# Kernel optimization log

Hardware: AMD Instinct MI355X
Metric: run time of the kernel (lower is better)

The kernel has to match this reference:

```python
import jax, jax.numpy as jnp
import numpy as np
from jax import lax

V, D, H, K, B, T = 32000, 300, 300, 9, 64, 512


def _lstm_dir(x, w_ih, w_hh, b_ih, b_hh, h0, c0):
    # x: [B, T, D]; torch gate order: i, f, g, o
    def step(carry, xt):
        h, c = carry
        gates = xt @ w_ih.T + h @ w_hh.T + b_ih + b_hh  # [B, 4H]
        i, f, g, o = jnp.split(gates, 4, axis=-1)
        i, f, o = jax.nn.sigmoid(i), jax.nn.sigmoid(f), jax.nn.sigmoid(o)
        g = jnp.tanh(g)
        c = f * c + i * g
        h = o * jnp.tanh(c)
        return (h, c), h

    xs = jnp.transpose(x, (1, 0, 2))  # [T, B, D]
    _, hs = lax.scan(step, (h0, c0), xs)
    return jnp.transpose(hs, (1, 0, 2))  # [B, T, H]


def _emissions(tokens, emb, w_ih_f, w_hh_f, b_ih_f, b_hh_f,
               w_ih_b, w_hh_b, b_ih_b, b_hh_b, h0, c0, w_out, b_out):
    x = emb[tokens]  # [B, T, D]
    hf = _lstm_dir(x, w_ih_f, w_hh_f, b_ih_f, b_hh_f, h0[0], c0[0])
    hb = _lstm_dir(jnp.flip(x, axis=1), w_ih_b, w_hh_b, b_ih_b, b_hh_b, h0[1], c0[1])
    hb = jnp.flip(hb, axis=1)
    out = jnp.concatenate([hf, hb], axis=-1)  # [B, T, 2H]
    return out @ w_out.T + b_out  # [B, T, K]


def _crf_nll(emissions, tags, mask, start_t, end_t, trans):
    # torchcrf: -sum_b log p(tags | emissions)
    e = jnp.transpose(emissions, (1, 0, 2))  # [T, B, K]
    tg = tags.T                               # [T, B]
    m = mask.T.astype(emissions.dtype)        # [T, B]
    bidx = jnp.arange(tags.shape[0])
    # numerator: gold path score
    num = start_t[tg[0]] + e[0][bidx, tg[0]]
    def nstep(carry, inp):
        et, tt, tp, mt = inp
        return carry + (trans[tp, tt] + et[bidx, tt]) * mt, None
    num, _ = lax.scan(nstep, num, (e[1:], tg[1:], tg[:-1], m[1:]))
    last_idx = mask.sum(axis=1).astype(jnp.int32) - 1
    last_tags = tags[bidx, last_idx]
    num = num + end_t[last_tags]
    # denominator: forward algorithm
    alpha = start_t + e[0]  # [B, K]
    def dstep(alpha, inp):
        et, mt = inp
        nxt = jax.scipy.special.logsumexp(alpha[:, :, None] + trans[None], axis=1) + et
        return jnp.where(mt[:, None] > 0, nxt, alpha), None
    alpha, _ = lax.scan(dstep, alpha, (e[1:], m[1:]))
    den = jax.scipy.special.logsumexp(alpha + end_t, axis=1)
    return -jnp.sum(num - den)


def _viterbi(emissions, mask, start_t, end_t, trans):
    e = jnp.transpose(emissions, (1, 0, 2))  # [T, B, K]
    m = mask.T                               # [T, B]
    score = start_t + e[0]                   # [B, K]
    def fstep(score, inp):
        et, mt = inp
        br = score[:, :, None] + trans[None]  # [B, K_prev, K_next]
        best = br.max(axis=1)
        idx = br.argmax(axis=1).astype(jnp.int32)  # [B, K]
        new = best + et
        return jnp.where(mt[:, None], new, score), idx
    score, history = lax.scan(fstep, score, (e[1:], m[1:]))  # history: [T-1, B, K]
    score = score + end_t
    last = jnp.argmax(score, axis=-1).astype(jnp.int32)  # [B]
    def bstep(tag, inp):
        idx_t, mt = inp
        prev = jnp.take_along_axis(idx_t, tag[:, None], axis=1)[:, 0]
        tag = jnp.where(mt, prev, tag)
        return tag, tag
    _, tags_rev = lax.scan(bstep, last, (history, m[1:]), reverse=True)  # [T-1, B]
    path = jnp.concatenate([tags_rev, last[None]], axis=0)  # [T, B]
    return path.T  # [B, T]


def setup_inputs() -> dict:
    key = jax.random.key(0)
    ks = jax.random.split(key, 20)
    s = 0.1
    emb = jax.random.normal(ks[0], (V, D), jnp.float32) * s
    emb = emb.at[0].set(0.0)  # padding_idx row
    inp = {
        "tokens": jax.random.randint(ks[1], (B, T), 0, V, jnp.int32),
        "tags": jax.random.randint(ks[2], (B, T), 0, K, jnp.int32),
        "mask": jnp.ones((B, T), jnp.bool_),
        "emb": emb,
        "w_ih_f": jax.random.normal(ks[3], (4 * H, D), jnp.float32) * s,
        "w_hh_f": jax.random.normal(ks[4], (4 * H, H), jnp.float32) * s,
        "b_ih_f": jax.random.normal(ks[5], (4 * H,), jnp.float32) * s,
        "b_hh_f": jax.random.normal(ks[6], (4 * H,), jnp.float32) * s,
        "w_ih_b": jax.random.normal(ks[7], (4 * H, D), jnp.float32) * s,
        "w_hh_b": jax.random.normal(ks[8], (4 * H, H), jnp.float32) * s,
        "b_ih_b": jax.random.normal(ks[9], (4 * H,), jnp.float32) * s,
        "b_hh_b": jax.random.normal(ks[10], (4 * H,), jnp.float32) * s,
        "h0": jax.random.normal(ks[11], (2, B, H), jnp.float32),
        "c0": jax.random.normal(ks[12], (2, B, H), jnp.float32),
        "w_out": jax.random.normal(ks[13], (K, 2 * H), jnp.float32) * s,
        "b_out": jax.random.normal(ks[14], (K,), jnp.float32) * s,
        "start_t": jax.random.normal(ks[15], (K,), jnp.float32) * s,
        "end_t": jax.random.normal(ks[16], (K,), jnp.float32) * s,
        "trans": jax.random.normal(ks[17], (K, K), jnp.float32) * s,
    }
    return inp


def reference(tokens, tags, mask, emb, w_ih_f, w_hh_f, b_ih_f, b_hh_f,
              w_ih_b, w_hh_b, b_ih_b, b_hh_b, h0, c0, w_out, b_out,
              start_t, end_t, trans):
    feats = _emissions(tokens, emb, w_ih_f, w_hh_f, b_ih_f, b_hh_f,
                       w_ih_b, w_hh_b, b_ih_b, b_hh_b, h0, c0, w_out, b_out)
    paths = _viterbi(feats, mask, start_t, end_t, trans)
    loss = _crf_nll(feats, tags, mask, start_t, end_t, trans)
    return paths, loss
```

## Files before the change

### kernel.cpp

```cpp
#include <hip/hip_runtime.h>
#include <math.h>

#define NV 32000
#define ND 300
#define NH 300
#define NK 9
#define NB 64
#define NT 512

typedef short bf16x8 __attribute__((ext_vector_type(8)));
typedef float f32x4  __attribute__((ext_vector_type(4)));

__device__ inline short bf16r(float x) {
    return (short)((__float_as_uint(x) + 0x8000u) >> 16);
}

__device__ inline float tanh_fast(float x) {
    float e2 = __expf(2.f * x);
    return 1.f - 2.f / (e2 + 1.f);
}

__device__ inline void bar_lds() {
    asm volatile("s_waitcnt lgkmcnt(0)" ::: "memory");
    __builtin_amdgcn_s_barrier();
    asm volatile("" ::: "memory");
}

#define WB_OFF   0ull
#define WB_F     768000ull
#define E_OFF    (WB_OFF + WB_F)
#define E_SZ     ((unsigned long long)NT*NB*NK)
#define CBUF_OFF (E_OFF + E_SZ)
#define CBUF_SZ  (2ull*NB*NH)
#define HSLOT_OFF (CBUF_OFF + CBUF_SZ)
#define HSLOT_SZ  (2ull*2*NB*NH)
#define XP_OFF   (HSLOT_OFF + HSLOT_SZ)
#define XPC_SZ   (2ull*64*1200*64)

__global__ __launch_bounds__(256) void k_wcvt(
    const float* __restrict__ wihf, const float* __restrict__ wihb,
    const float* __restrict__ whhf, const float* __restrict__ whhb,
    short* __restrict__ dst)
{
    int i = blockIdx.x*256 + threadIdx.x;
    if (i >= 1536000) return;
    int d  = i / 384000;
    int r2 = i % 384000;
    int j  = r2 / 320, k = r2 % 320;
    const float* src = (d == 0) ? wihf : (d == 1) ? wihb : (d == 2) ? whhf : whhb;
    float v = (k < 300) ? src[(size_t)j*300 + k] : 0.f;
    dst[i] = bf16r(v);
}

__global__ __launch_bounds__(256) void k_xproj(
    const int* __restrict__ tokens, const float* __restrict__ emb,
    const short* __restrict__ wb16,
    const float* __restrict__ bif, const float* __restrict__ bhf,
    const float* __restrict__ bib, const float* __restrict__ bhb,
    float* __restrict__ xpc, int chunk)
{
    const int tid = threadIdx.x;
    const int w  = tid >> 6, L = tid & 63;
    const int lm = L & 15, lq = L >> 4;
    const int dir = blockIdx.z;
    const int m0 = blockIdx.x*128 + w*32;
    const int n0 = blockIdx.y*80;
    const int tbase = dir ? (448 - chunk*64) : (chunk*64);

    const float* arow[2];
#pragma unroll
    for (int mi = 0; mi < 2; ++mi) {
        int m = m0 + mi*16 + lm;
        int b = m >> 6, lt = m & 63;
        arow[mi] = emb + (size_t)tokens[b*512 + tbase + lt] * 300;
    }
    const short* brow[5];
#pragma unroll
    for (int ni = 0; ni < 5; ++ni) {
        int j = n0 + ni*16 + lm;
        brow[ni] = wb16 + ((size_t)dir*1200 + j)*320;
    }

    f32x4 acc[2][5];
#pragma unroll
    for (int mi = 0; mi < 2; ++mi)
#pragma unroll
        for (int ni = 0; ni < 5; ++ni)
#pragma unroll
            for (int r = 0; r < 4; ++r) acc[mi][ni][r] = 0.f;

    const float4 z4 = make_float4(0.f,0.f,0.f,0.f);
    for (int k0 = 0; k0 < 320; k0 += 32) {
        const int kk = k0 + lq*8;
        bf16x8 af[2], bf[5];
#pragma unroll
        for (int mi = 0; mi < 2; ++mi) {
            float4 f1 = (kk   < 300) ? *(const float4*)(arow[mi] + kk)     : z4;
            float4 f2 = (kk+4 < 300) ? *(const float4*)(arow[mi] + kk + 4) : z4;
            af[mi][0]=bf16r(f1.x); af[mi][1]=bf16r(f1.y); af[mi][2]=bf16r(f1.z); af[mi][3]=bf16r(f1.w);
            af[mi][4]=bf16r(f2.x); af[mi][5]=bf16r(f2.y); af[mi][6]=bf16r(f2.z); af[mi][7]=bf16r(f2.w);
        }
#pragma unroll
        for (int ni = 0; ni < 5; ++ni)
            bf[ni] = *(const bf16x8*)(brow[ni] + kk);
#pragma unroll
        for (int mi = 0; mi < 2; ++mi)
#pragma unroll
            for (int ni = 0; ni < 5; ++ni)
                acc[mi][ni] = __builtin_amdgcn_mfma_f32_16x16x32_bf16(
                                  af[mi], bf[ni], acc[mi][ni], 0, 0, 0);
    }

#pragma unroll
    for (int ni = 0; ni < 5; ++ni) {
        int j = n0 + ni*16 + lm;
        int g = j/300, rr = j%300;
        int slc = rr/20, ul = rr%20;
        float bias = dir ? (bib[j]+bhb[j]) : (bif[j]+bhf[j]);
#pragma unroll
        for (int mi = 0; mi < 2; ++mi) {
#pragma unroll
            for (int r = 0; r < 4; ++r) {
                int m = m0 + mi*16 + lq*4 + r;
                int b = m >> 6, lt = m & 63;
                int sp = dir ? (63 - lt) : lt;
                size_t idx = ((((size_t)dir*64 + sp)*8 + (b>>3))*15 + slc)*640
                           + (size_t)(b&7)*80 + g*20 + ul;
                xpc[idx] = acc[mi][ni][r] + bias;
            }
        }
    }
}

__global__ __launch_bounds__(256) void k_rnn(
    const float* __restrict__ xpc,
    const short* __restrict__ whh16,
    const float* __restrict__ h0,
    unsigned* hslot, float* __restrict__ cbuf,
    float* __restrict__ ev, const float* __restrict__ wout,
    int s_begin, int s_count, int full)
{
    extern __shared__ char lds_pad[];
    __shared__ __align__(16) short h_sh16[16*328];
    __shared__ __align__(16) float xp_sh[640];
    __shared__ __align__(16) float gates_sh[80*9];
    __shared__ __align__(16) float wo_sh[180];
    __shared__ __align__(16) float hloc[160];
    __shared__ __align__(16) float ev_loc[64*72];
    (void)lds_pad;

    const int tid = threadIdx.x;
    const int wv  = tid >> 6, L = tid & 63;
    const int lm  = L & 15, lq = L >> 4;
    const int dir = blockIdx.x / 120;
    const int rem = blockIdx.x % 120;
    const int sl  = rem / 8;
    const int gb  = rem % 8;
    const int u0  = sl * 20;

    const int tb = (wv == 0) ? 0 : (wv + 1);
    const int tn = (wv == 0) ? 2 : 1;

    bf16x8 A[2][10];
#pragma unroll 2
    for (int mt = 0; mt < 2; ++mt) {
        if (mt < tn) {
            int r = (tb + mt)*16 + lm;
            int grow = (r/20)*300 + u0 + (r%20);
            const short* wr = whh16 + ((size_t)dir*1200 + grow)*320;
#pragma unroll
            for (int ks = 0; ks < 10; ++ks)
                A[mt][ks] = *(const bf16x8*)(wr + ks*32 + lq*8);
        }
    }
    if (tid < 180) wo_sh[tid] = wout[(tid/20)*600 + dir*300 + u0 + (tid%20)];

    for (int i = tid; i < 16*328; i += 256) h_sh16[i] = 0;

    const bool isPW = (tid < 160);
    const int bl_p = tid/20, lu_p = tid%20;
    float c_reg = 0.f;
    if (isPW) c_reg = cbuf[((size_t)dir*NB + gb*8 + bl_p)*NH + u0 + lu_p];

    auto xaddr = [&](int s) -> const float* {
        const float* xb; int sp;
        if (full) { xb = xpc + (size_t)(s >> 6)*XPC_SZ; sp = s & 63; }
        else      { xb = xpc;                            sp = s - s_begin; }
        return xb + ((((size_t)dir*64 + sp)*8 + gb)*15 + sl)*640 + (size_t)tid*4;
    };
    float4 xpr;
    if (tid < 160) xpr = *(const float4*)xaddr(s_begin);

    bar_lds();

    for (int s = s_begin; s < s_begin + s_count; ++s) {
        unsigned vb[10];
        unsigned* hsrc = hslot + (((size_t)(s & 1)*2 + dir)*NB + gb*8)*NH;
        if (s > 0 && tid < 240) {
#pragma unroll
            for (int j = 0; j < 10; ++j) {
                int i = tid + 256*j;
                if (i < 2400)
                    vb[j] = __hip_atomic_load(hsrc + i, __ATOMIC_RELAXED,
                                              __HIP_MEMORY_SCOPE_AGENT);
            }
        }

        if (tid < 160) *(float4*)(&xp_sh[tid*4]) = xpr;
        if (tid < 160 && (s + 1) < s_begin + s_count)
            xpr = *(const float4*)xaddr(s + 1);

        if (s == 0) {
            const float* h0p = h0 + ((size_t)dir*NB + gb*8)*NH;
            for (int i = tid; i < 2400; i += 256)
                h_sh16[(i/300)*328 + (i%300)] = bf16r(h0p[i]);
        } else if (tid < 240) {
            const unsigned tg = (unsigned)s & 0xFFFFu;
            bool ok = false;
            while (!ok) {
                ok = true;
#pragma unroll
                for (int j = 0; j < 10; ++j) {
                    int i = tid + 256*j;
                    if (i < 2400 && (vb[j] >> 16) != tg) {
                        ok = false;
                        vb[j] = __hip_atomic_load(hsrc + i, __ATOMIC_RELAXED,
                                                  __HIP_MEMORY_SCOPE_AGENT);
                    }
                }
            }
#pragma unroll
            for (int j = 0; j < 10; ++j) {
                int i = tid + 256*j;
                if (i < 2400)
                    h_sh16[(i/300)*328 + (i%300)] = (short)(vb[j] & 0xFFFFu);
            }
        }
        bar_lds();

        {
            bf16x8 Bf[10];
#pragma unroll
            for (int ks = 0; ks < 10; ++ks)
                Bf[ks] = *(const bf16x8*)(h_sh16 + lm*328 + ks*32 + lq*8);
            f32x4 acc0, acc1;
#pragma unroll 2
            for (int mt = 0; mt < 2; ++mt) {
                if (mt < tn) {
#pragma unroll
                    for (int r = 0; r < 4; ++r) { acc0[r] = 0.f; acc1[r] = 0.f; }
#pragma unroll
                    for (int ks = 0; ks < 5; ++ks)
                        acc0 = __builtin_amdgcn_mfma_f32_16x16x32_bf16(
                                   A[mt][ks], Bf[ks], acc0, 0, 0, 0);
#pragma unroll
                    for (int ks = 5; ks < 10; ++ks)
                        acc1 = __builtin_amdgcn_mfma_f32_16x16x32_bf16(
                                   A[mt][ks], Bf[ks], acc1, 0, 0, 0);
                    if (lm < 8) {
#pragma unroll
                        for (int r = 0; r < 4; ++r)
                            gates_sh[((tb+mt)*16 + lq*4 + r)*9 + lm] = acc0[r] + acc1[r];
                    }
                }
            }
        }
        bar_lds();

        if (isPW) {
            float G[4];
#pragma unroll
            for (int g = 0; g < 4; ++g)
                G[g] = xp_sh[bl_p*80 + g*20 + lu_p] + gates_sh[(g*20 + lu_p)*9 + bl_p];
            float ig = 1.f/(1.f+__expf(-G[0]));
            float fg = 1.f/(1.f+__expf(-G[1]));
            float gg = tanh_fast(G[2]);
            float og = 1.f/(1.f+__expf(-G[3]));
            c_reg = fg*c_reg + ig*gg;
            float h = og*tanh_fast(c_reg);
            unsigned hb = (__float_as_uint(h) + 0x8000u) >> 16;
            unsigned pk = (((unsigned)(s+1) & 0xFFFFu) << 16) | hb;
            __hip_atomic_store(
                &hslot[(((size_t)((s+1)&1)*2 + dir)*NB + gb*8 + bl_p)*NH + u0 + lu_p],
                pk, __ATOMIC_RELAXED, __HIP_MEMORY_SCOPE_AGENT);
            hloc[bl_p*20 + lu_p] = h;
        }
        bar_lds();

        const int widx = (s - s_begin) & 63;
        if (tid < 72) {
            int b = tid/9, k = tid%9;
            float a = 0.f;
#pragma unroll
            for (int u = 0; u < 20; ++u) a += hloc[b*20+u]*wo_sh[k*20+u];
            ev_loc[widx*72 + tid] = a;
        }

        if (widx == 63) {
            bar_lds();
            const int sbase = s - 63;
            for (int i = tid; i < 64*72; i += 256) {
                int wi = i / 72, j = i % 72;
                int bb = j / 9, kk = j % 9;
                int tt = dir ? (511 - (sbase + wi)) : (sbase + wi);
                atomicAdd(&ev[((size_t)tt*NB + gb*8 + bb)*NK + kk], ev_loc[i]);
            }
        }
    }

    if (isPW) cbuf[((size_t)dir*NB + gb*8 + bl_p)*NH + u0 + lu_p] = c_reg;
}

#define BT_C 14
#define BT_L 37

__global__ __launch_bounds__(128) void k_crf(
    const float* __restrict__ ev, const int* __restrict__ tags,
    const float* __restrict__ start_t, const float* __restrict__ end_t,
    const float* __restrict__ trans, const float* __restrict__ bout,
    float* __restrict__ out)
{
    __shared__ __align__(16) float ex_a[12];
    __shared__ __align__(16) float ex_v[12];
    __shared__ int hist_sh[511*NK];
    __shared__ int fmap[BT_C*NK];
    __shared__ int entry_sh[BT_C];
    __shared__ int last_sh;

    const int b = blockIdx.x, tid = threadIdx.x;
    const int wv = tid >> 6, ln = tid & 63;

    if (wv == 0) {
        float part = 0.f;
        for (int t = ln; t < NT; t += 64) {
            int tc = tags[b*NT + t];
            float e = ev[((size_t)t*NB + b)*NK + tc] + bout[tc];
            float pre = (t == 0) ? start_t[tc] : trans[tags[b*NT + t - 1]*9 + tc];
            part += pre + e;
        }
        if (ln == 63) part += end_t[tags[b*NT + NT - 1]];
#pragma unroll
        for (int off = 32; off > 0; off >>= 1)
            part += __shfl_down(part, off, 64);
        const float num = part;

        if (ln < 9) {
            const int kc = ln;
            float Tc[9];
#pragma unroll
            for (int kp = 0; kp < 9; ++kp) Tc[kp] = __expf(trans[kp*9 + kc]);
            const float bo = bout[kc];
            ex_a[kc] = start_t[kc] + ev[(size_t)b*NK + kc] + bo;
            float etn = ev[((size_t)1*NB + b)*NK + kc] + bo;

            for (int t = 1; t < NT; ++t) {
                float et = etn;
                if (t + 1 < NT) etn = ev[((size_t)(t+1)*NB + b)*NK + kc] + bo;

                float4 s0 = *(const float4*)(&ex_a[0]);
                float4 s1 = *(const float4*)(&ex_a[4]);
                float  a8 = ex_a[8];
                float a0=s0.x,a1=s0.y,a2=s0.z,a3=s0.w,a4=s1.x,a5=s1.y,a6=s1.z,a7=s1.w;

                float M = fmaxf(fmaxf(fmaxf(a0,a1),fmaxf(a2,a3)),
                                fmaxf(fmaxf(a4,a5),fmaxf(a6,a7)));
                M = fmaxf(M, a8);
                float s =        __expf(a0-M)*Tc[0];
                s = fmaf(__expf(a1-M), Tc[1], s);
                s = fmaf(__expf(a2-M), Tc[2], s);
                s = fmaf(__expf(a3-M), Tc[3], s);
                s = fmaf(__expf(a4-M), Tc[4], s);
                s = fmaf(__expf(a5-M), Tc[5], s);
                s = fmaf(__expf(a6-M), Tc[6], s);
                s = fmaf(__expf(a7-M), Tc[7], s);
                s = fmaf(__expf(a8-M), Tc[8], s);
                ex_a[kc] = M + __logf(s) + et;
            }

            if (ln == 0) {
                float M = -1e30f;
#pragma unroll
                for (int k = 0; k < 9; ++k) M = fmaxf(M, ex_a[k] + end_t[k]);
                float ls = 0.f;
#pragma unroll
                for (int k = 0; k < 9; ++k) ls += __expf(ex_a[k] + end_t[k] - M);
                float den = M + __logf(ls);
                atomicAdd(out + NB*NT, den - num);
            }
        }
    } else {
        if (ln < 9) {
            const int kc = ln;
            float Tc[9];
#pragma unroll
            for (int kp = 0; kp < 9; ++kp) Tc[kp] = trans[kp*9 + kc];
            const float bo = bout[kc];
            ex_v[kc] = start_t[kc] + ev[(size_t)b*NK + kc] + bo;
            float etn = ev[((size_t)1*NB + b)*NK + kc] + bo;

            for (int t = 1; t < NT; ++t) {
                float et = etn;
                if (t + 1 < NT) etn = ev[((size_t)(t+1)*NB + b)*NK + kc] + bo;

                float4 s0 = *(const float4*)(&ex_v[0]);
                float4 s1 = *(const float4*)(&ex_v[4]);
                float  a8 = ex_v[8];
                float a0=s0.x,a1=s0.y,a2=s0.z,a3=s0.w,a4=s1.x,a5=s1.y,a6=s1.z,a7=s1.w;

                float bv = a0 + Tc[0]; int arg = 0;
                float v;
                v = a1+Tc[1]; if (v > bv) { bv = v; arg = 1; }
                v = a2+Tc[2]; if (v > bv) { bv = v; arg = 2; }
                v = a3+Tc[3]; if (v > bv) { bv = v; arg = 3; }
                v = a4+Tc[4]; if (v > bv) { bv = v; arg = 4; }
                v = a5+Tc[5]; if (v > bv) { bv = v; arg = 5; }
                v = a6+Tc[6]; if (v > bv) { bv = v; arg = 6; }
                v = a7+Tc[7]; if (v > bv) { bv = v; arg = 7; }
                v = a8+Tc[8]; if (v > bv) { bv = v; arg = 8; }
                hist_sh[(t-1)*NK + kc] = arg;
                ex_v[kc] = bv + et;
            }

            if (ln == 0) {
                float best = -1e30f; int last = 0;
#pragma unroll
                for (int k = 0; k < 9; ++k) {
                    float v = ex_v[k] + end_t[k];
                    if (v > best) { best = v; last = k; }
                }
                last_sh = last;
            }
        }
    }

    __syncthreads();

    if (tid < BT_C*NK) {
        int c = tid / NK, s = tid % NK;
        int lo = c*BT_L, hi = min(511, lo + BT_L);
        int pos = s;
        for (int i = hi - 1; i >= lo; --i) pos = hist_sh[i*NK + pos];
        fmap[c*NK + s] = pos;
    }
    __syncthreads();
    if (tid == 0) {
        int e = last_sh;
        entry_sh[BT_C-1] = e;
        for (int c = BT_C - 2; c >= 0; --c) {
            e = fmap[(c+1)*NK + e];
            entry_sh[c] = e;
        }
    }
    __syncthreads();
    int* pout = (int*)out;
    if (tid < BT_C) {
        int c = tid;
        int lo = c*BT_L, hi = min(511, lo + BT_L);
        int pos = entry_sh[c];
        for (int i = hi - 1; i >= lo; --i) {
            pos = hist_sh[i*NK + pos];
            pout[b*NT + i] = pos;
        }
    }
    if (tid == 0) pout[b*NT + NT - 1] = last_sh;
}

extern "C" void kernel_launch(void* const* d_in, const int* in_sizes, int n_in,
                              void* d_out, int out_size, void* d_ws, size_t ws_size,
                              hipStream_t stream)
{
    (void)in_sizes; (void)n_in;

    const int*   tokens = (const int*)  d_in[0];
    const int*   tags   = (const int*)  d_in[1];
    const float* emb    = (const float*)d_in[3];
    const float* wihf   = (const float*)d_in[4];
    const float* whhf   = (const float*)d_in[5];
    const float* bihf   = (const float*)d_in[6];
    const float* bhhf   = (const float*)d_in[7];
    const float* wihb   = (const float*)d_in[8];
    const float* whhb   = (const float*)d_in[9];
    const float* bib    = (const float*)d_in[10];
    const float* bhhb   = (const float*)d_in[11];
    const float* h0     = (const float*)d_in[12];
    const float* c0     = (const float*)d_in[13];
    const float* wout   = (const float*)d_in[14];
    const float* bout   = (const float*)d_in[15];
    const float* startt = (const float*)d_in[16];
    const float* endt   = (const float*)d_in[17];
    const float* trans  = (const float*)d_in[18];

    float* ws    = (float*)d_ws;
    short* wb16  = (short*)(ws + WB_OFF);
    short* whh16 = wb16 + 768000;
    float* evp   = ws + E_OFF;
    float* cbuf  = ws + CBUF_OFF;
    unsigned* hslot = (unsigned*)(ws + HSLOT_OFF);
    float* xp    = ws + XP_OFF;
    float* out   = (float*)d_out;

    const size_t need_full = (XP_OFF + 8ull*XPC_SZ) * 4ull;
    const bool full = (ws_size >= need_full);

    (void)hipMemsetAsync(d_out, 0, (size_t)out_size * sizeof(float), stream);
    (void)hipMemsetAsync(evp, 0, (size_t)E_SZ * sizeof(float), stream);
    (void)hipMemcpyAsync(cbuf, c0, 2ull*NB*NH*sizeof(float), hipMemcpyDeviceToDevice, stream);

    k_wcvt<<<6000, 256, 0, stream>>>(wihf, wihb, whhf, whhb, wb16);

    if (full) {
        for (int c = 0; c < 8; ++c)
            k_xproj<<<dim3(32, 15, 2), 256, 0, stream>>>(
                tokens, emb, wb16, bihf, bhhf, bib, bhhb, xp + (size_t)c*XPC_SZ, c);
        k_rnn<<<240, 256, 81920, stream>>>(
            xp, whh16, h0, hslot, cbuf, evp, wout, 0, 512, 1);
    } else {
        for (int c = 0; c < 8; ++c) {
            k_xproj<<<dim3(32, 15, 2), 256, 0, stream>>>(
                tokens, emb, wb16, bihf, bhhf, bib, bhhb, xp, c);
            k_rnn<<<240, 256, 81920, stream>>>(
                xp, whh16, h0, hslot, cbuf, evp, wout, c*64, 64, 0);
        }
    }
    k_crf<<<64, 128, 0, stream>>>(evp, tags, startt, endt, trans, bout, out);
}
```

Before: 2.005 ms.

## Pre-convert embeddings to bf16 and always run chunked xproj/rnn launches

Adds a kernel converting the full embedding table to padded bf16 so the input projection loads bf16 rows directly instead of converting fp32 on the fly. The recurrent kernel is simplified: it always runs in 64-step chunks interleaved with projection launches, drops the xp register prefetch and the 80KB dynamic LDS padding, and emits emissions via per-step atomics instead of batched LDS staging. This trades conversion cost and more launches/atomics for simpler code and reduced per-element conversion work.

```diff
diff --git a/kernel.cpp b/kernel.cpp
--- a/kernel.cpp
+++ b/kernel.cpp
@@ -18,12 +18,6 @@
 __device__ inline float tanh_fast(float x) {
     float e2 = __expf(2.f * x);
     return 1.f - 2.f / (e2 + 1.f);
-}
-
-__device__ inline void bar_lds() {
-    asm volatile("s_waitcnt lgkmcnt(0)" ::: "memory");
-    __builtin_amdgcn_s_barrier();
-    asm volatile("" ::: "memory");
 }
 
 #define WB_OFF   0ull
@@ -36,6 +30,9 @@
 #define HSLOT_SZ  (2ull*2*NB*NH)
 #define XP_OFF   (HSLOT_OFF + HSLOT_SZ)
 #define XPC_SZ   (2ull*64*1200*64)
+#define EB_OFF   (XP_OFF + XPC_SZ)
+#define EB_SZ    (32000ull*320/2)
+#define WS_NEED_EB ((EB_OFF + EB_SZ)*4ull)
 
 __global__ __launch_bounds__(256) void k_wcvt(
     const float* __restrict__ wihf, const float* __restrict__ wihb,
@@ -52,8 +49,19 @@
     dst[i] = bf16r(v);
 }
 
+__global__ __launch_bounds__(256) void k_ecvt(
+    const float* __restrict__ emb, short* __restrict__ dst)
+{
+    int i = blockIdx.x*256 + threadIdx.x;
+    if (i >= 32000*320) return;
+    int row = i / 320, col = i % 320;
+    float v = (col < 300) ? emb[(size_t)row*300 + col] : 0.f;
+    dst[i] = bf16r(v);
+}
+
 __global__ __launch_bounds__(256) void k_xproj(
     const int* __restrict__ tokens, const float* __restrict__ emb,
+    const short* __restrict__ eb16, int use_eb,
     const short* __restrict__ wb16,
     const float* __restrict__ bif, const float* __restrict__ bhf,
     const float* __restrict__ bib, const float* __restrict__ bhb,
@@ -67,12 +75,12 @@
     const int n0 = blockIdx.y*80;
     const int tbase = dir ? (448 - chunk*64) : (chunk*64);
 
-    const float* arow[2];
+    int tok[2];
 #pragma unroll
     for (int mi = 0; mi < 2; ++mi) {
         int m = m0 + mi*16 + lm;
         int b = m >> 6, lt = m & 63;
-        arow[mi] = emb + (size_t)tokens[b*512 + tbase + lt] * 300;
+        tok[mi] = tokens[b*512 + tbase + lt];
     }
     const short* brow[5];
 #pragma unroll
@@ -89,26 +97,51 @@
 #pragma unroll
             for (int r = 0; r < 4; ++r) acc[mi][ni][r] = 0.f;
 
-    const float4 z4 = make_float4(0.f,0.f,0.f,0.f);
-    for (int k0 = 0; k0 < 320; k0 += 32) {
-        const int kk = k0 + lq*8;
-        bf16x8 af[2], bf[5];
-#pragma unroll
-        for (int mi = 0; mi < 2; ++mi) {
-            float4 f1 = (kk   < 300) ? *(const float4*)(arow[mi] + kk)     : z4;
-            float4 f2 = (kk+4 < 300) ? *(const float4*)(arow[mi] + kk + 4) : z4;
-            af[mi][0]=bf16r(f1.x); af[mi][1]=bf16r(f1.y); af[mi][2]=bf16r(f1.z); af[mi][3]=bf16r(f1.w);
-            af[mi][4]=bf16r(f2.x); af[mi][5]=bf16r(f2.y); af[mi][6]=bf16r(f2.z); af[mi][7]=bf16r(f2.w);
-        }
-#pragma unroll
-        for (int ni = 0; ni < 5; ++ni)
-            bf[ni] = *(const bf16x8*)(brow[ni] + kk);
-#pragma unroll
-        for (int mi = 0; mi < 2; ++mi)
+    if (use_eb) {
+        const short* arow[2];
+#pragma unroll
+        for (int mi = 0; mi < 2; ++mi) arow[mi] = eb16 + (size_t)tok[mi]*320;
+        for (int k0 = 0; k0 < 320; k0 += 32) {
+            const int kk = k0 + lq*8;
+            bf16x8 af[2], bf[5];
+#pragma unroll
+            for (int mi = 0; mi < 2; ++mi)
+                af[mi] = *(const bf16x8*)(arow[mi] + kk);
 #pragma unroll
             for (int ni = 0; ni < 5; ++ni)
-                acc[mi][ni] = __builtin_amdgcn_mfma_f32_16x16x32_bf16(
-                                  af[mi], bf[ni], acc[mi][ni], 0, 0, 0);
+                bf[ni] = *(const bf16x8*)(brow[ni] + kk);
+#pragma unroll
+            for (int mi = 0; mi < 2; ++mi)
+#pragma unroll
+                for (int ni = 0; ni < 5; ++ni)
+                    acc[mi][ni] = __builtin_amdgcn_mfma_f32_16x16x32_bf16(
+                                      af[mi], bf[ni], acc[mi][ni], 0, 0, 0);
+        }
+    } else {
+        const float* arow[2];
+#pragma unroll
+        for (int mi = 0; mi < 2; ++mi) arow[mi] = emb + (size_t)tok[mi]*300;
+        const float4 z4 = make_float4(0.f,0.f,0.f,0.f);
+        for (int k0 = 0; k0 < 320; k0 += 32) {
+            const int kk = k0 + lq*8;
+            bf16x8 af[2], bf[5];
+#pragma unroll
+            for (int mi = 0; mi < 2; ++mi) {
+                float4 f1 = (kk   < 300) ? *(const float4*)(arow[mi] + kk)     : z4;
+                float4 f2 = (kk+4 < 300) ? *(const float4*)(arow[mi] + kk + 4) : z4;
+                af[mi][0]=bf16r(f1.x); af[mi][1]=bf16r(f1.y); af[mi][2]=bf16r(f1.z); af[mi][3]=bf16r(f1.w);
+                af[mi][4]=bf16r(f2.x); af[mi][5]=bf16r(f2.y); af[mi][6]=bf16r(f2.z); af[mi][7]=bf16r(f2.w);
+            }
+#pragma unroll
+            for (int ni = 0; ni < 5; ++ni)
+                bf[ni] = *(const bf16x8*)(brow[ni] + kk);
+#pragma unroll
+            for (int mi = 0; mi < 2; ++mi)
+#pragma unroll
+                for (int ni = 0; ni < 5; ++ni)
+                    acc[mi][ni] = __builtin_amdgcn_mfma_f32_16x16x32_bf16(
+                                      af[mi], bf[ni], acc[mi][ni], 0, 0, 0);
+        }
     }
 
 #pragma unroll
@@ -138,16 +171,13 @@
     const float* __restrict__ h0,
     unsigned* hslot, float* __restrict__ cbuf,
     float* __restrict__ ev, const float* __restrict__ wout,
-    int s_begin, int s_count, int full)
+    int s_begin, int s_count)
 {
-    extern __shared__ char lds_pad[];
     __shared__ __align__(16) short h_sh16[16*328];
     __shared__ __align__(16) float xp_sh[640];
     __shared__ __align__(16) float gates_sh[80*9];
     __shared__ __align__(16) float wo_sh[180];
     __shared__ __align__(16) float hloc[160];
-    __shared__ __align__(16) float ev_loc[64*72];
-    (void)lds_pad;
 
     const int tid = threadIdx.x;
     const int wv  = tid >> 6, L = tid & 63;
@@ -182,18 +212,12 @@
     float c_reg = 0.f;
     if (isPW) c_reg = cbuf[((size_t)dir*NB + gb*8 + bl_p)*NH + u0 + lu_p];
 
-    auto xaddr = [&](int s) -> const float* {
-        const float* xb; int sp;
-        if (full) { xb = xpc + (size_t)(s >> 6)*XPC_SZ; sp = s & 63; }
-        else      { xb = xpc;                            sp = s - s_begin; }
-        return xb + ((((size_t)dir*64 + sp)*8 + gb)*15 + sl)*640 + (size_t)tid*4;
-    };
-    float4 xpr;
-    if (tid < 160) xpr = *(const float4*)xaddr(s_begin);
-
-    bar_lds();
+    __syncthreads();
 
     for (int s = s_begin; s < s_begin + s_count; ++s) {
+        const int t = dir ? (511 - s) : s;
+        const int sp = s - s_begin;
+
         unsigned vb[10];
         unsigned* hsrc = hslot + (((size_t)(s & 1)*2 + dir)*NB + gb*8)*NH;
         if (s > 0 && tid < 240) {
@@ -206,9 +230,10 @@
             }
         }
 
-        if (tid < 160) *(float4*)(&xp_sh[tid*4]) = xpr;
-        if (tid < 160 && (s + 1) < s_begin + s_count)
-            xpr = *(const float4*)xaddr(s + 1);
+        {
+            const float* xsrc = xpc + ((((size_t)dir*64 + sp)*8 + gb)*15 + sl)*640;
+            if (tid < 160) *(float4*)(&xp_sh[tid*4]) = *(const float4*)(xsrc + tid*4);
+        }
 
         if (s == 0) {
             const float* h0p = h0 + ((size_t)dir*NB + gb*8)*NH;
@@ -236,36 +261,32 @@
                     h_sh16[(i/300)*328 + (i%300)] = (short)(vb[j] & 0xFFFFu);
             }
         }
-        bar_lds();
+        __syncthreads();
 
         {
             bf16x8 Bf[10];
 #pragma unroll
             for (int ks = 0; ks < 10; ++ks)
                 Bf[ks] = *(const bf16x8*)(h_sh16 + lm*328 + ks*32 + lq*8);
-            f32x4 acc0, acc1;
+            f32x4 acc[2];
 #pragma unroll 2
             for (int mt = 0; mt < 2; ++mt) {
                 if (mt < tn) {
 #pragma unroll
-                    for (int r = 0; r < 4; ++r) { acc0[r] = 0.f; acc1[r] = 0.f; }
-#pragma unroll
-                    for (int ks = 0; ks < 5; ++ks)
-                        acc0 = __builtin_amdgcn_mfma_f32_16x16x32_bf16(
-                                   A[mt][ks], Bf[ks], acc0, 0, 0, 0);
-#pragma unroll
-                    for (int ks = 5; ks < 10; ++ks)
-                        acc1 = __builtin_amdgcn_mfma_f32_16x16x32_bf16(
-                                   A[mt][ks], Bf[ks], acc1, 0, 0, 0);
+                    for (int r = 0; r < 4; ++r) acc[mt][r] = 0.f;
+#pragma unroll
+                    for (int ks = 0; ks < 10; ++ks)
+                        acc[mt] = __builtin_amdgcn_mfma_f32_16x16x32_bf16(
+                                      A[mt][ks], Bf[ks], acc[mt], 0, 0, 0);
                     if (lm < 8) {
 #pragma unroll
                         for (int r = 0; r < 4; ++r)
-                            gates_sh[((tb+mt)*16 + lq*4 + r)*9 + lm] = acc0[r] + acc1[r];
+                            gates_sh[((tb+mt)*16 + lq*4 + r)*9 + lm] = acc[mt][r];
                     }
                 }
             }
         }
-        bar_lds();
+        __syncthreads();
 
         if (isPW) {
             float G[4];
@@ -285,26 +306,14 @@
                 pk, __ATOMIC_RELAXED, __HIP_MEMORY_SCOPE_AGENT);
             hloc[bl_p*20 + lu_p] = h;
         }
-        bar_lds();
-
-        const int widx = (s - s_begin) & 63;
+        __syncthreads();
+
         if (tid < 72) {
             int b = tid/9, k = tid%9;
             float a = 0.f;
 #pragma unroll
             for (int u = 0; u < 20; ++u) a += hloc[b*20+u]*wo_sh[k*20+u];
-            ev_loc[widx*72 + tid] = a;
-        }
-
-        if (widx == 63) {
-            bar_lds();
-            const int sbase = s - 63;
-            for (int i = tid; i < 64*72; i += 256) {
-                int wi = i / 72, j = i % 72;
-                int bb = j / 9, kk = j % 9;
-                int tt = dir ? (511 - (sbase + wi)) : (sbase + wi);
-                atomicAdd(&ev[((size_t)tt*NB + gb*8 + bb)*NK + kk], ev_loc[i]);
-            }
+            atomicAdd(&ev[((size_t)t*NB + gb*8 + b)*NK + k], a);
         }
     }
 
@@ -497,30 +506,24 @@
     float* cbuf  = ws + CBUF_OFF;
     unsigned* hslot = (unsigned*)(ws + HSLOT_OFF);
     float* xp    = ws + XP_OFF;
+    short* eb16  = (short*)(ws + EB_OFF);
     float* out   = (float*)d_out;
 
-    const size_t need_full = (XP_OFF + 8ull*XPC_SZ) * 4ull;
-    const bool full = (ws_size >= need_full);
+    const int use_eb = (ws_size >= WS_NEED_EB) ? 1 : 0;
 
     (void)hipMemsetAsync(d_out, 0, (size_t)out_size * sizeof(float), stream);
     (void)hipMemsetAsync(evp, 0, (size_t)E_SZ * sizeof(float), stream);
     (void)hipMemcpyAsync(cbuf, c0, 2ull*NB*NH*sizeof(float), hipMemcpyDeviceToDevice, stream);
 
     k_wcvt<<<6000, 256, 0, stream>>>(wihf, wihb, whhf, whhb, wb16);
-
-    if (full) {
-        for (int c = 0; c < 8; ++c)
-            k_xproj<<<dim3(32, 15, 2), 256, 0, stream>>>(
-                tokens, emb, wb16, bihf, bhhf, bib, bhhb, xp + (size_t)c*XPC_SZ, c);
-        k_rnn<<<240, 256, 81920, stream>>>(
-            xp, whh16, h0, hslot, cbuf, evp, wout, 0, 512, 1);
-    } else {
-        for (int c = 0; c < 8; ++c) {
-            k_xproj<<<dim3(32, 15, 2), 256, 0, stream>>>(
-                tokens, emb, wb16, bihf, bhhf, bib, bhhb, xp, c);
-            k_rnn<<<240, 256, 81920, stream>>>(
-                xp, whh16, h0, hslot, cbuf, evp, wout, c*64, 64, 0);
-        }
+    if (use_eb)
+        k_ecvt<<<40000, 256, 0, stream>>>(emb, eb16);
+
+    for (int c = 0; c < 8; ++c) {
+        k_xproj<<<dim3(32, 15, 2), 256, 0, stream>>>(
+            tokens, emb, eb16, use_eb, wb16, bihf, bhhf, bib, bhhb, xp, c);
+        k_rnn<<<240, 256, 0, stream>>>(
+            xp, whh16, h0, hslot, cbuf, evp, wout, c*64, 64);
     }
     k_crf<<<64, 128, 0, stream>>>(evp, tags, startt, endt, trans, bout, out);
 }
```

New measurement: 1.876 ms. -6.5%, faster.
